# Kernel tuning notes

Measured on AMD Instinct MI355X. Metric: run time of the kernel, lower is better.

Reference implementation:

```python
import jax, jax.numpy as jnp
import numpy as np

B, N, D = 2, 2048, 1024
H = 16                      # num_heads, head_dim = 64
E, K, CF = 4, 2, 1.0        # num_experts, top_k, capacity_factor
MLP_H = int(D * 4.0)        # dense Mlp hidden (mlp_ratio=4.0)
MOE_H = int(D * 0.25)       # expert hidden (hard-coded dim*0.25 in source)


def setup_inputs() -> dict:
    key = jax.random.key(0)
    ks = jax.random.split(key, 12)
    r = lambda k, shp, s=0.02: jax.random.normal(k, shp, jnp.float32) * s
    return dict(
        x=jax.random.normal(ks[0], (B, N, D), jnp.float32),
        noise=jax.random.normal(ks[1], (B, N, E), jnp.float32),
        ln1_g=jnp.ones((D,), jnp.float32), ln1_b=jnp.zeros((D,), jnp.float32),
        ln2_g=jnp.ones((D,), jnp.float32), ln2_b=jnp.zeros((D,), jnp.float32),
        w_qkv=r(ks[2], (3 * D, D)),
        w_proj=r(ks[3], (D, D)), b_proj=jnp.zeros((D,), jnp.float32),
        w_route=r(ks[4], (D, E), 0.05), b_route=jnp.zeros((E,), jnp.float32),
        w_noise=r(ks[5], (D, E), 0.05), b_noise=jnp.zeros((E,), jnp.float32),
        we1=r(ks[6], (E, D, MOE_H)), be1=jnp.zeros((E, MOE_H), jnp.float32),
        we2=r(ks[7], (E, MOE_H, D)), be2=jnp.zeros((E, D), jnp.float32),
        w_mlp1=r(ks[8], (D, MLP_H)), b_mlp1=jnp.zeros((MLP_H,), jnp.float32),
        w_mlp2=r(ks[9], (MLP_H, D)), b_mlp2=jnp.zeros((D,), jnp.float32),
    )


def _ln(x, g, b, eps=1e-5):
    mu = x.mean(-1, keepdims=True)
    var = ((x - mu) ** 2).mean(-1, keepdims=True)
    return (x - mu) * jax.lax.rsqrt(var + eps) * g + b


def _gelu(x):
    return jax.nn.gelu(x, approximate=False)  # torch nn.GELU default (erf)


def reference(x, noise, ln1_g, ln1_b, ln2_g, ln2_b, w_qkv, w_proj, b_proj,
              w_route, b_route, w_noise, b_noise, we1, be1, we2, be2,
              w_mlp1, b_mlp1, w_mlp2, b_mlp2):
    Bs, Ns, Ds = x.shape
    hd = Ds // H
    # --- attention branch ---
    x1 = _ln(x, ln1_g, ln1_b)
    qkv = (x1 @ w_qkv.T).reshape(Bs, Ns, 3, H, hd).transpose(2, 0, 3, 1, 4)
    q, k, v = qkv[0] * (hd ** -0.5), qkv[1], qkv[2]
    attn = jax.nn.softmax(jnp.einsum('bhnd,bhmd->bhnm', q, k), axis=-1)
    ao = jnp.einsum('bhnm,bhmd->bhnd', attn, v).transpose(0, 2, 1, 3).reshape(Bs, Ns, Ds)
    x = x + (ao @ w_proj.T + b_proj)
    # --- shared norm for mlp + moe ---
    x2 = _ln(x, ln2_g, ln2_b)
    # --- noisy top-k router ---
    logits = x2 @ w_route + b_route                  # [B,N,E]
    noisy = logits + noise * jax.nn.softplus(x2 @ w_noise + b_noise)
    topv, topi = jax.lax.top_k(noisy, K)             # [B,N,K]
    probs = jax.nn.softmax(topv, axis=-1)            # softmax over sparse logits == softmax over top-k
    T = Bs * Ns
    flat_x = x2.reshape(T, Ds)
    fidx = topi.reshape(T, K)
    rows = jnp.arange(T)[:, None]
    gate = jnp.zeros((T, E), noisy.dtype).at[rows, fidx].set(probs.reshape(T, K))
    capacity = int(T * K / E * CF)
    # --- capacity-limited dispatch / expert MLP / combine ---
    def dispatch(eid, W1, b1, W2, b2):
        mask = jnp.any(fidx == eid, axis=-1)                     # [T]
        order = jnp.argsort(jnp.logical_not(mask))               # stable: selected tokens first, in token order
        sel = order[:capacity]                                   # [C]
        valid = mask[sel].astype(flat_x.dtype)
        h = _gelu(flat_x[sel] @ W1 + b1)
        out = h @ W2 + b2
        w = gate[sel, eid] * valid
        return sel, out * w[:, None]
    sel, outw = jax.vmap(dispatch)(jnp.arange(E), we1, be1, we2, be2)   # [E,C], [E,C,D]
    moe = jnp.zeros_like(flat_x).at[sel.reshape(-1)].add(outw.reshape(-1, Ds)).reshape(Bs, Ns, Ds)
    # --- dense mlp branch ---
    mlp = _gelu(x2 @ w_mlp1 + b_mlp1) @ w_mlp2 + b_mlp2
    return x + mlp + moe
```

## Files before the change

kernel.cpp:

```cpp
#include <hip/hip_runtime.h>
#include <hip/hip_bf16.h>
#include <math.h>

typedef __bf16 bf16;
typedef __bf16 bf16x4 __attribute__((ext_vector_type(4)));
typedef __bf16 bf16x8 __attribute__((ext_vector_type(8)));
typedef float  f32x4  __attribute__((ext_vector_type(4)));
typedef short  s16x4  __attribute__((ext_vector_type(4)));

#define T_TOK 4096
#define DIM   1024
#define NHEAD 16
#define SEQ   2048
#define NEXP  4
#define CAP   2048
#define MLPH  4096
#define MOEH  256

__device__ __forceinline__ float gelu_exact(float v) {
    return 0.5f * v * (1.f + erff(v * 0.70710678118654752f));
}

struct HL { bf16 h, l; };
__device__ __forceinline__ HL split2(float v) {
    HL r; r.h = (bf16)v; r.l = (bf16)(v - (float)r.h); return r;
}

__device__ __forceinline__ float fast_exp2(float x) {
#if __has_builtin(__builtin_amdgcn_exp2f)
    return __builtin_amdgcn_exp2f(x);
#else
    return exp2f(x);
#endif
}

__device__ __forceinline__ f32x4 mfma16(bf16x4 a, bf16x4 b, f32x4 c) {
    return __builtin_amdgcn_mfma_f32_16x16x16bf16_1k(
        __builtin_bit_cast(s16x4, a), __builtin_bit_cast(s16x4, b), c, 0, 0, 0);
}

__device__ __forceinline__ void gload16(const bf16* gptr, bf16* lptr) {
    __builtin_amdgcn_global_load_lds(
        (const __attribute__((address_space(1))) unsigned int*)gptr,
        (__attribute__((address_space(3))) unsigned int*)lptr,
        16, 0, 0);
}

__global__ __launch_bounds__(256)
void ln_split_kernel(const float* __restrict__ x, const float* __restrict__ g,
                     const float* __restrict__ b, bf16* __restrict__ oh, bf16* __restrict__ ol) {
    int wave = threadIdx.x >> 6, lane = threadIdx.x & 63;
    long t = (long)blockIdx.x * 4 + wave;
    const float* xr = x + t * DIM;
    float v[16];
    #pragma unroll
    for (int i = 0; i < 16; i++) v[i] = xr[i * 64 + lane];
    float s = 0.f, s2 = 0.f;
    #pragma unroll
    for (int i = 0; i < 16; i++) { s += v[i]; s2 += v[i] * v[i]; }
    #pragma unroll
    for (int m = 1; m < 64; m <<= 1) { s += __shfl_xor(s, m); s2 += __shfl_xor(s2, m); }
    float mu  = s * (1.f / DIM);
    float var = s2 * (1.f / DIM) - mu * mu;
    float rs  = 1.f / sqrtf(var + 1e-5f);
    #pragma unroll
    for (int i = 0; i < 16; i++) {
        int d = i * 64 + lane;
        HL sp = split2((v[i] - mu) * rs * g[d] + b[d]);
        oh[t * DIM + d] = sp.h; ol[t * DIM + d] = sp.l;
    }
}

__global__ __launch_bounds__(256)
void ln_kernel(const float* __restrict__ x, const float* __restrict__ g,
               const float* __restrict__ b, bf16* __restrict__ out) {
    int wave = threadIdx.x >> 6, lane = threadIdx.x & 63;
    long t = (long)blockIdx.x * 4 + wave;
    const float* xr = x + t * DIM;
    float v[16];
    #pragma unroll
    for (int i = 0; i < 16; i++) v[i] = xr[i * 64 + lane];
    float s = 0.f, s2 = 0.f;
    #pragma unroll
    for (int i = 0; i < 16; i++) { s += v[i]; s2 += v[i] * v[i]; }
    #pragma unroll
    for (int m = 1; m < 64; m <<= 1) { s += __shfl_xor(s, m); s2 += __shfl_xor(s2, m); }
    float mu  = s * (1.f / DIM);
    float var = s2 * (1.f / DIM) - mu * mu;
    float rs  = 1.f / sqrtf(var + 1e-5f);
    #pragma unroll
    for (int i = 0; i < 16; i++) {
        int d = i * 64 + lane;
        out[t * DIM + d] = (bf16)((v[i] - mu) * rs * g[d] + b[d]);
    }
}

__global__ __launch_bounds__(256)
void split_pair_kernel(const float* __restrict__ in, bf16* __restrict__ h, bf16* __restrict__ l) {
    long i0 = ((long)blockIdx.x * 256 + threadIdx.x) * 4;
    f32x4 v = *(const f32x4*)&in[i0];
    bf16x4 vh, vl;
    #pragma unroll
    for (int j = 0; j < 4; j++) { HL sp = split2(v[j]); vh[j] = sp.h; vl[j] = sp.l; }
    *(bf16x4*)&h[i0] = vh; *(bf16x4*)&l[i0] = vl;
}

__global__ __launch_bounds__(256)
void transpose_conv_kernel(const float* __restrict__ in, bf16* __restrict__ out, int R, int C) {
    __shared__ bf16 tile[32][33];
    long bo = (long)blockIdx.z * R * C;
    in += bo; out += bo;
    int c0 = blockIdx.x * 32, r0 = blockIdx.y * 32;
    int tx = threadIdx.x & 31, ty = threadIdx.x >> 5;
    #pragma unroll
    for (int i = 0; i < 32; i += 8)
        tile[ty + i][tx] = (bf16)in[(long)(r0 + ty + i) * C + c0 + tx];
    __syncthreads();
    #pragma unroll
    for (int i = 0; i < 32; i += 8)
        out[(long)(c0 + ty + i) * R + r0 + tx] = tile[tx][ty + i];
}

__global__ __launch_bounds__(256)
void gemm_qkv(const bf16* __restrict__ Ah_g, const bf16* __restrict__ Al_g,
              const bf16* __restrict__ Bh_g, const bf16* __restrict__ Bl_g,
              bf16* __restrict__ Qh_g, bf16* __restrict__ Ql_g,
              bf16* __restrict__ Kh_g, bf16* __restrict__ Kl_g,
              bf16* __restrict__ VtH, bf16* __restrict__ VtL) {
    const int K = DIM;
    __shared__ alignas(16) bf16 Ah[8192], Al[8192], Bh[8192], Bl[8192];
    int tid = threadIdx.x;
    int wave = tid >> 6, lane = tid & 63;
    int l16 = lane & 15, l4 = lane >> 4;
    int wr = (wave >> 1) * 64, wc = (wave & 1) * 64;
    int row0 = blockIdx.y * 128, col0 = blockIdx.x * 128;
    int colb = (lane & 7) * 8;
    f32x4 acc[4][4] = {};
    for (int k0 = 0; k0 < K; k0 += 64) {
        #pragma unroll
        for (int p = 0; p < 4; p++) {
            int rl = p * 32 + wave * 8 + (lane >> 3);
            int lb = p * 2048 + wave * 512;
            gload16(&Ah_g[(long)(row0 + rl) * K + k0 + colb], &Ah[lb]);
            gload16(&Al_g[(long)(row0 + rl) * K + k0 + colb], &Al[lb]);
            gload16(&Bh_g[(long)(col0 + rl) * K + k0 + colb], &Bh[lb]);
            gload16(&Bl_g[(long)(col0 + rl) * K + k0 + colb], &Bl[lb]);
        }
        __syncthreads();
        #pragma unroll
        for (int ks = 0; ks < 2; ks++) {
            bf16x8 ah[4], al[4], bh[4], bl[4];
            #pragma unroll
            for (int i = 0; i < 4; i++) {
                ah[i] = *(const bf16x8*)&Ah[(wr + i*16 + l16)*64 + ks*32 + l4*8];
                al[i] = *(const bf16x8*)&Al[(wr + i*16 + l16)*64 + ks*32 + l4*8];
            }
            #pragma unroll
            for (int j = 0; j < 4; j++) {
                bh[j] = *(const bf16x8*)&Bh[(wc + j*16 + l16)*64 + ks*32 + l4*8];
                bl[j] = *(const bf16x8*)&Bl[(wc + j*16 + l16)*64 + ks*32 + l4*8];
            }
            #pragma unroll
            for (int i = 0; i < 4; i++)
                #pragma unroll
                for (int j = 0; j < 4; j++) {
                    acc[i][j] = __builtin_amdgcn_mfma_f32_16x16x32_bf16(ah[i], bh[j], acc[i][j], 0, 0, 0);
                    acc[i][j] = __builtin_amdgcn_mfma_f32_16x16x32_bf16(ah[i], bl[j], acc[i][j], 0, 0, 0);
                    acc[i][j] = __builtin_amdgcn_mfma_f32_16x16x32_bf16(al[i], bh[j], acc[i][j], 0, 0, 0);
                }
        }
        __syncthreads();
    }
    if (col0 < 2048) {
        bf16* oh = (col0 < 1024) ? Qh_g : Kh_g;
        bf16* ol = (col0 < 1024) ? Ql_g : Kl_g;
        float qscale = (col0 < 1024) ? 0.18033688011112043f : 1.0f;
        #pragma unroll
        for (int i = 0; i < 4; i++)
            #pragma unroll
            for (int r = 0; r < 4; r++) {
                int t = row0 + wr + i * 16 + l4 * 4 + r;
                int bq = t >> 11, s = t & 2047;
                #pragma unroll
                for (int j = 0; j < 4; j++) {
                    int col = (col0 + wc + j * 16 + l16) & 1023;
                    int hh = col >> 6, dl = col & 63;
                    long o = ((long)(bq * NHEAD + hh) * SEQ + s) * 64 + dl;
                    HL sp = split2(acc[i][j][r] * qscale);
                    oh[o] = sp.h; ol[o] = sp.l;
                }
            }
    } else {
        #pragma unroll
        for (int i = 0; i < 4; i++) {
            int s0 = row0 + wr + i * 16 + l4 * 4;
            int b = s0 >> 11, sl = s0 & 2047;
            #pragma unroll
            for (int j = 0; j < 4; j++) {
                int d = col0 - 2048 + wc + j * 16 + l16;
                int h = d >> 6, dl = d & 63;
                long base = ((long)(b * NHEAD + h) * 64 + dl) * SEQ + (sl ^ ((dl & 1) << 2));
                bf16x4 vh, vl;
                #pragma unroll
                for (int r = 0; r < 4; r++) { HL sp = split2(acc[i][j][r]); vh[r] = sp.h; vl[r] = sp.l; }
                *(bf16x4*)&VtH[base] = vh;
                *(bf16x4*)&VtL[base] = vl;
            }
        }
    }
}

__device__ __forceinline__ bf16x8 sw_frag(const bf16* arr, int row, int cc) {
    return *(const bf16x8*)&arr[row * 64 + ((cc ^ (row & 7)) * 8)];
}
__device__ __forceinline__ bf16x4 v_frag(const bf16* arr, int d, int q) {
    return *(const bf16x4*)&arr[d * 64 + ((q ^ (d & 15)) * 4)];
}

__global__ __launch_bounds__(512, 4)
void flash_attn(const bf16* __restrict__ Qh_g, const bf16* __restrict__ Ql_g,
                const bf16* __restrict__ Kh_g, const bf16* __restrict__ Kl_g,
                const bf16* __restrict__ VtH_g, const bf16* __restrict__ VtL_g,
                bf16* __restrict__ aoh, bf16* __restrict__ aol) {
    __shared__ alignas(16) bf16 KhS[2][4096], KlS[2][4096], VhS[2][4096], VlS[2][4096];
    int tid = threadIdx.x;
    int wave = tid >> 6, lane = tid & 63;
    int l16 = lane & 15, l4 = lane >> 4;
    int bid = blockIdx.x;
    int bh = bid & 31;
    int b = bh >> 4, h = bh & 15;
    int q0 = (bid >> 5) * 128;

    bf16x8 qfh[2], qfl[2];
    {
        const bf16* qh = Qh_g + ((long)bh * SEQ + q0 + wave * 16 + l16) * 64;
        const bf16* ql = Ql_g + ((long)bh * SEQ + q0 + wave * 16 + l16) * 64;
        #pragma unroll
        for (int ks = 0; ks < 2; ks++) {
            qfh[ks] = *(const bf16x8*)&qh[ks * 32 + l4 * 8];
            qfl[ks] = *(const bf16x8*)&ql[ks * 32 + l4 * 8];
        }
    }
    int r8 = lane >> 3;
    int c8 = lane & 7;
    const bf16* kh_g = Kh_g + (long)bh * SEQ * 64;
    const bf16* kl_g = Kl_g + (long)bh * SEQ * 64;
    const bf16* vh_g = VtH_g + (long)bh * 64 * SEQ;
    const bf16* vl_g = VtL_g + (long)bh * 64 * SEQ;

    float m_s = -1e30f, l_s = 0.f;
    f32x4 accO[4] = {};

    auto stage = [&](int c0, int bsel) {
        int R0 = wave * 8;
        int row = R0 + r8;
        int ksw = (c8 ^ r8) * 8;
        int vsw = (c8 ^ ((wave * 4 + (r8 >> 1)) & 7)) * 8;
        gload16(&kh_g[(long)(c0 + row) * 64 + ksw], &KhS[bsel][R0 * 64]);
        gload16(&kl_g[(long)(c0 + row) * 64 + ksw], &KlS[bsel][R0 * 64]);
        gload16(&vh_g[(long)row * SEQ + c0 + vsw], &VhS[bsel][R0 * 64]);
        gload16(&vl_g[(long)row * SEQ + c0 + vsw], &VlS[bsel][R0 * 64]);
    };

    auto compute = [&](const bf16* KhT, const bf16* KlT, const bf16* VhT, const bf16* VlT) {
        f32x4 st[4] = {};
        __builtin_amdgcn_s_setprio(1);
        #pragma unroll
        for (int ks = 0; ks < 2; ks++) {
            #pragma unroll
            for (int i = 0; i < 4; i++) {
                bf16x8 akh = sw_frag(KhT, i * 16 + l16, ks * 4 + l4);
                bf16x8 akl = sw_frag(KlT, i * 16 + l16, ks * 4 + l4);
                st[i] = __builtin_amdgcn_mfma_f32_16x16x32_bf16(akh, qfh[ks], st[i], 0, 0, 0);
                st[i] = __builtin_amdgcn_mfma_f32_16x16x32_bf16(akl, qfh[ks], st[i], 0, 0, 0);
                st[i] = __builtin_amdgcn_mfma_f32_16x16x32_bf16(akh, qfl[ks], st[i], 0, 0, 0);
            }
        }
        __builtin_amdgcn_s_setprio(0);
        float mx = st[0][0];
        #pragma unroll
        for (int i = 0; i < 4; i++)
            #pragma unroll
            for (int r = 0; r < 4; r++) mx = fmaxf(mx, st[i][r]);
        mx = fmaxf(mx, __shfl_xor(mx, 16));
        mx = fmaxf(mx, __shfl_xor(mx, 32));
        if (!__all(mx <= m_s + 8.f)) {
            float mnew = fmaxf(m_s, mx);
            float alpha = fast_exp2(m_s - mnew);
            l_s *= alpha;
            #pragma unroll
            for (int i = 0; i < 4; i++)
                #pragma unroll
                for (int r = 0; r < 4; r++) accO[i][r] *= alpha;
            m_s = mnew;
        }
        float psum = 0.f;
        bf16x4 ph[4], pl[4];
        #pragma unroll
        for (int kb = 0; kb < 4; kb++)
            #pragma unroll
            for (int r = 0; r < 4; r++) {
                float pv = fast_exp2(st[kb][r] - m_s);
                psum += pv;
                HL sp = split2(pv);
                ph[kb][r] = sp.h; pl[kb][r] = sp.l;
            }
        psum += __shfl_xor(psum, 16);
        psum += __shfl_xor(psum, 32);
        l_s += psum;
        __builtin_amdgcn_s_setprio(1);
        #pragma unroll
        for (int kb = 0; kb < 4; kb++) {
            #pragma unroll
            for (int i = 0; i < 4; i++) {
                bf16x4 avh = v_frag(VhT, i * 16 + l16, kb * 4 + l4);
                bf16x4 avl = v_frag(VlT, i * 16 + l16, kb * 4 + l4);
                accO[i] = mfma16(avh, ph[kb], accO[i]);
                accO[i] = mfma16(avh, pl[kb], accO[i]);
                accO[i] = mfma16(avl, ph[kb], accO[i]);
            }
        }
        __builtin_amdgcn_s_setprio(0);
    };

    const int NT = SEQ / 64;
    stage(0, 0);
    #pragma unroll 1
    for (int t = 0; t < NT; t += 2) {
        stage((t + 1) * 64, 1);
        asm volatile("s_waitcnt vmcnt(4)" ::: "memory");
        __builtin_amdgcn_sched_barrier(0);
        __builtin_amdgcn_s_barrier();
        compute(KhS[0], KlS[0], VhS[0], VlS[0]);
        asm volatile("" ::: "memory");
        __builtin_amdgcn_s_barrier();
        if (t + 2 < NT) {
            stage((t + 2) * 64, 0);
            asm volatile("s_waitcnt vmcnt(4)" ::: "memory");
        } else {
            asm volatile("s_waitcnt vmcnt(0)" ::: "memory");
        }
        __builtin_amdgcn_sched_barrier(0);
        __builtin_amdgcn_s_barrier();
        compute(KhS[1], KlS[1], VhS[1], VlS[1]);
        asm volatile("" ::: "memory");
        __builtin_amdgcn_s_barrier();
    }

    float inv = 1.f / l_s;
    int q = q0 + wave * 16 + l16;
    #pragma unroll
    for (int i = 0; i < 4; i++) {
        bf16x4 oh4, ol4;
        #pragma unroll
        for (int r = 0; r < 4; r++) { HL sp = split2(accO[i][r] * inv); oh4[r] = sp.h; ol4[r] = sp.l; }
        long o = ((long)(b * SEQ + q)) * DIM + h * 64 + i * 16 + l4 * 4;
        *(bf16x4*)&aoh[o] = oh4;
        *(bf16x4*)&aol[o] = ol4;
    }
}

__global__ __launch_bounds__(256)
void gemm_proj(const bf16* __restrict__ Ah_g, const bf16* __restrict__ Al_g,
               const bf16* __restrict__ Bh_g, const bf16* __restrict__ Bl_g,
               const float* __restrict__ bias, const float* __restrict__ res,
               float* __restrict__ C, int N, int K) {
    __shared__ alignas(16) bf16 Ah[8192], Al[8192], Bh[8192], Bl[8192];
    int tid = threadIdx.x;
    int wave = tid >> 6, lane = tid & 63;
    int l16 = lane & 15, l4 = lane >> 4;
    int wr = (wave >> 1) * 64, wc = (wave & 1) * 64;
    int row0 = blockIdx.y * 128, col0 = blockIdx.x * 128;
    int colb = (lane & 7) * 8;
    f32x4 acc[4][4] = {};
    for (int k0 = 0; k0 < K; k0 += 64) {
        #pragma unroll
        for (int p = 0; p < 4; p++) {
            int rl = p * 32 + wave * 8 + (lane >> 3);
            int lb = p * 2048 + wave * 512;
            gload16(&Ah_g[(long)(row0 + rl) * K + k0 + colb], &Ah[lb]);
            gload16(&Al_g[(long)(row0 + rl) * K + k0 + colb], &Al[lb]);
            gload16(&Bh_g[(long)(col0 + rl) * K + k0 + colb], &Bh[lb]);
            gload16(&Bl_g[(long)(col0 + rl) * K + k0 + colb], &Bl[lb]);
        }
        __syncthreads();
        #pragma unroll
        for (int ks = 0; ks < 2; ks++) {
            bf16x8 ah[4], al[4], bh[4], bl[4];
            #pragma unroll
            for (int i = 0; i < 4; i++) {
                ah[i] = *(const bf16x8*)&Ah[(wr + i*16 + l16)*64 + ks*32 + l4*8];
                al[i] = *(const bf16x8*)&Al[(wr + i*16 + l16)*64 + ks*32 + l4*8];
            }
            #pragma unroll
            for (int j = 0; j < 4; j++) {
                bh[j] = *(const bf16x8*)&Bh[(wc + j*16 + l16)*64 + ks*32 + l4*8];
                bl[j] = *(const bf16x8*)&Bl[(wc + j*16 + l16)*64 + ks*32 + l4*8];
            }
            #pragma unroll
            for (int i = 0; i < 4; i++)
                #pragma unroll
                for (int j = 0; j < 4; j++) {
                    acc[i][j] = __builtin_amdgcn_mfma_f32_16x16x32_bf16(ah[i], bh[j], acc[i][j], 0, 0, 0);
                    acc[i][j] = __builtin_amdgcn_mfma_f32_16x16x32_bf16(ah[i], bl[j], acc[i][j], 0, 0, 0);
                    acc[i][j] = __builtin_amdgcn_mfma_f32_16x16x32_bf16(al[i], bh[j], acc[i][j], 0, 0, 0);
                }
        }
        __syncthreads();
    }
    #pragma unroll
    for (int i = 0; i < 4; i++)
        #pragma unroll
        for (int r = 0; r < 4; r++) {
            int grow = row0 + wr + i * 16 + l4 * 4 + r;
            #pragma unroll
            for (int j = 0; j < 4; j++) {
                int gcol = col0 + wc + j * 16 + l16;
                long o = (long)grow * N + gcol;
                C[o] = acc[i][j][r] + bias[gcol] + res[o];
            }
        }
}

template<bool BIAS, bool GELU, bool GATHER, int OUT_MODE>
__global__ __launch_bounds__(256)
void gemm_bt(const bf16* __restrict__ A, const bf16* __restrict__ Bt,
             const float* __restrict__ bias,
             bf16* __restrict__ Cbf, float* __restrict__ Cf,
             const int* __restrict__ rowmap, const float* __restrict__ roww,
             int M, int N, int K,
             long eA, long eB, long ebias, long eMap, long eC) {
    int ez = blockIdx.z;
    A += (long)ez * eA; Bt += (long)ez * eB;
    if (BIAS) bias += (long)ez * ebias;
    if (GATHER || OUT_MODE == 3) rowmap += (long)ez * eMap;
    if (OUT_MODE == 3) roww += (long)ez * eMap;
    if (OUT_MODE == 0) Cbf += (long)ez * eC;

    __shared__ alignas(16) bf16 As[8192];
    __shared__ alignas(16) bf16 Bs[8192];
    int tid = threadIdx.x;
    int wave = tid >> 6, lane = tid & 63;
    int l16 = lane & 15, l4 = lane >> 4;
    int wr = (wave >> 1) * 64, wc = (wave & 1) * 64;
    int row0 = blockIdx.y * 128, col0 = blockIdx.x * 128;
    int colb = (lane & 7) * 8;

    long arow[4];
    #pragma unroll
    for (int p = 0; p < 4; p++) {
        long gr = row0 + p * 32 + wave * 8 + (lane >> 3);
        if (GATHER) gr = rowmap[gr];
        arow[p] = gr;
    }
    f32x4 acc[4][4] = {};
    for (int k0 = 0; k0 < K; k0 += 64) {
        #pragma unroll
        for (int p = 0; p < 4; p++) {
            int rl = p * 32 + wave * 8 + (lane >> 3);
            int lb = p * 2048 + wave * 512;
            gload16(&A[arow[p] * K + k0 + colb], &As[lb]);
            gload16(&Bt[(long)(col0 + rl) * K + k0 + colb], &Bs[lb]);
        }
        __syncthreads();
        #pragma unroll
        for (int ks = 0; ks < 2; ks++) {
            bf16x8 af[4], bfr[4];
            #pragma unroll
            for (int i = 0; i < 4; i++) af[i]  = *(const bf16x8*)&As[(wr + i*16 + l16)*64 + ks*32 + l4*8];
            #pragma unroll
            for (int j = 0; j < 4; j++) bfr[j] = *(const bf16x8*)&Bs[(wc + j*16 + l16)*64 + ks*32 + l4*8];
            #pragma unroll
            for (int i = 0; i < 4; i++)
                #pragma unroll
                for (int j = 0; j < 4; j++)
                    acc[i][j] = __builtin_amdgcn_mfma_f32_16x16x32_bf16(af[i], bfr[j], acc[i][j], 0, 0, 0);
        }
        __syncthreads();
    }
    #pragma unroll
    for (int i = 0; i < 4; i++)
        #pragma unroll
        for (int r = 0; r < 4; r++) {
            int grow = row0 + wr + i * 16 + l4 * 4 + r;
            int st = 0; float sw = 0.f;
            if (OUT_MODE == 3) { st = rowmap[grow]; sw = roww[grow]; }
            #pragma unroll
            for (int j = 0; j < 4; j++) {
                int gcol = col0 + wc + j * 16 + l16;
                float v = acc[i][j][r];
                if (BIAS) v += bias[gcol];
                if (GELU) v = gelu_exact(v);
                if (OUT_MODE == 0) {
                    Cbf[(long)grow * N + gcol] = (bf16)v;
                } else if (OUT_MODE == 2) {
                    long o = (long)grow * N + gcol;
                    Cf[o] += v;
                } else {
                    atomicAdd(&Cf[(long)st * N + gcol], sw * v);
                }
            }
        }
}

__global__ __launch_bounds__(256)
void routing_kernel(const float* __restrict__ xres, const float* __restrict__ g,
                    const float* __restrict__ b, const float* __restrict__ w_route,
                    const float* __restrict__ b_route, const float* __restrict__ w_noise,
                    const float* __restrict__ b_noise, const float* __restrict__ noise,
                    int* __restrict__ topi, float* __restrict__ topp) {
    int wave = threadIdx.x >> 6, lane = threadIdx.x & 63;
    long t = (long)blockIdx.x * 4 + wave;
    const float* xr = xres + t * DIM;
    float v[16];
    #pragma unroll
    for (int i = 0; i < 16; i++) v[i] = xr[i * 64 + lane];
    float s = 0.f, s2 = 0.f;
    #pragma unroll
    for (int i = 0; i < 16; i++) { s += v[i]; s2 += v[i] * v[i]; }
    #pragma unroll
    for (int m = 1; m < 64; m <<= 1) { s += __shfl_xor(s, m); s2 += __shfl_xor(s2, m); }
    float mu  = s * (1.f / DIM);
    float var = s2 * (1.f / DIM) - mu * mu;
    float rs  = 1.f / sqrtf(var + 1e-5f);
    float accr[4] = {0.f,0.f,0.f,0.f}, accn[4] = {0.f,0.f,0.f,0.f};
    #pragma unroll
    for (int i = 0; i < 16; i++) {
        int d = i * 64 + lane;
        float n = (v[i] - mu) * rs * g[d] + b[d];
        #pragma unroll
        for (int e = 0; e < 4; e++) {
            accr[e] += n * w_route[d * 4 + e];
            accn[e] += n * w_noise[d * 4 + e];
        }
    }
    #pragma unroll
    for (int e = 0; e < 4; e++)
        #pragma unroll
        for (int m = 1; m < 64; m <<= 1) {
            accr[e] += __shfl_xor(accr[e], m);
            accn[e] += __shfl_xor(accn[e], m);
        }
    if (lane == 0) {
        float nz[4];
        #pragma unroll
        for (int e = 0; e < 4; e++) {
            float logit = accr[e] + b_route[e];
            float si = accn[e] + b_noise[e];
            float sp = si > 0.f ? si + log1pf(expf(-si)) : log1pf(expf(si));
            nz[e] = logit + noise[t * 4 + e] * sp;
        }
        int i1 = 0;
        #pragma unroll
        for (int e = 1; e < 4; e++) if (nz[e] > nz[i1]) i1 = e;
        int i2 = -1; float v2 = -1e30f;
        #pragma unroll
        for (int e = 0; e < 4; e++) if (e != i1 && nz[e] > v2) { v2 = nz[e]; i2 = e; }
        float ex = expf(v2 - nz[i1]);
        topi[t * 2]     = i1; topi[t * 2 + 1] = i2;
        topp[t * 2]     = 1.f / (1.f + ex);
        topp[t * 2 + 1] = ex / (1.f + ex);
    }
}

__global__ __launch_bounds__(256)
void dispatch_kernel(const int* __restrict__ topi, const float* __restrict__ topp,
                     int* __restrict__ sel, float* __restrict__ wgt) {
    int e = threadIdx.x >> 6, lane = threadIdx.x & 63;
    int cnt = 0;
    for (int c = 0; c < T_TOK; c += 64) {
        int t = c + lane;
        int i0 = topi[t * 2], i1 = topi[t * 2 + 1];
        bool m = (i0 == e) || (i1 == e);
        unsigned long long bal = __ballot(m);
        int pos = cnt + __popcll(bal & ((1ull << lane) - 1ull));
        if (m && pos < CAP) {
            sel[e * CAP + pos] = t;
            wgt[e * CAP + pos] = (i0 == e) ? topp[t * 2] : topp[t * 2 + 1];
        }
        cnt += (int)__popcll(bal);
    }
    if (cnt > CAP) cnt = CAP;
    for (int pos = cnt + lane; pos < CAP; pos += 64) {
        sel[e * CAP + pos] = 0;
        wgt[e * CAP + pos] = 0.f;
    }
}

extern "C" void kernel_launch(void* const* d_in, const int* in_sizes, int n_in,
                              void* d_out, int out_size, void* d_ws, size_t ws_size,
                              hipStream_t stream) {
    (void)in_sizes; (void)n_in; (void)out_size; (void)ws_size;
    const float* x       = (const float*)d_in[0];
    const float* noise   = (const float*)d_in[1];
    const float* ln1_g   = (const float*)d_in[2];
    const float* ln1_b   = (const float*)d_in[3];
    const float* ln2_g   = (const float*)d_in[4];
    const float* ln2_b   = (const float*)d_in[5];
    const float* w_qkv   = (const float*)d_in[6];
    const float* w_proj  = (const float*)d_in[7];
    const float* b_proj  = (const float*)d_in[8];
    const float* w_route = (const float*)d_in[9];
    const float* b_route = (const float*)d_in[10];
    const float* w_noise = (const float*)d_in[11];
    const float* b_noise = (const float*)d_in[12];
    const float* we1     = (const float*)d_in[13];
    const float* be1     = (const float*)d_in[14];
    const float* we2     = (const float*)d_in[15];
    const float* be2     = (const float*)d_in[16];
    const float* w_mlp1  = (const float*)d_in[17];
    const float* b_mlp1  = (const float*)d_in[18];
    const float* w_mlp2  = (const float*)d_in[19];
    const float* b_mlp2  = (const float*)d_in[20];
    float* d_outf = (float*)d_out;

    const size_t MB = 1024 * 1024;
    char* ws = (char*)d_ws;
    bf16* x1h = (bf16*)(ws);
    bf16* x1l = (bf16*)(ws + 8 * MB);
    bf16* aoh = (bf16*)(ws);
    bf16* aol = (bf16*)(ws + 8 * MB);
    bf16* w_mlp1T = (bf16*)(ws);
    bf16* w_mlp2T = (bf16*)(ws + 8 * MB);
    bf16* wqkvh = (bf16*)(ws + 16 * MB);
    bf16* wqkvl = (bf16*)(ws + 22 * MB);
    bf16* we1T  = (bf16*)(ws + 16 * MB);
    bf16* we2T  = (bf16*)(ws + 18 * MB);
    bf16* h_e   = (bf16*)(ws + 20 * MB);
    bf16* wprojh = (bf16*)(ws + 28 * MB);
    bf16* wprojl = (bf16*)(ws + 30 * MB);
    bf16* Qh = (bf16*)(ws + 32 * MB);
    bf16* Ql = (bf16*)(ws + 40 * MB);
    bf16* Kh = (bf16*)(ws + 48 * MB);
    bf16* Kl = (bf16*)(ws + 56 * MB);
    bf16* h_mlp = (bf16*)(ws + 32 * MB);
    bf16*  VtH  = (bf16*)(ws + 64 * MB);
    bf16*  VtL  = (bf16*)(ws + 72 * MB);
    bf16*  x2b  = (bf16*)(ws + 64 * MB);
    int*   topi = (int*)(ws + 72 * MB);
    float* topp = (float*)(ws + 72 * MB + 32768);
    int*   sel  = (int*)(ws + 72 * MB + 65536);
    float* wgt  = (float*)(ws + 72 * MB + 98304);

    ln_split_kernel<<<T_TOK/4, 256, 0, stream>>>(x, ln1_g, ln1_b, x1h, x1l);
    split_pair_kernel<<<(3*DIM*DIM)/1024, 256, 0, stream>>>(w_qkv, wqkvh, wqkvl);
    split_pair_kernel<<<(DIM*DIM)/1024,   256, 0, stream>>>(w_proj, wprojh, wprojl);

    gemm_qkv<<<dim3(3*DIM/128, T_TOK/128), 256, 0, stream>>>(
        x1h, x1l, wqkvh, wqkvl, Qh, Ql, Kh, Kl, VtH, VtL);

    flash_attn<<<dim3(32 * (SEQ/128)), 512, 0, stream>>>(Qh, Ql, Kh, Kl, VtH, VtL, aoh, aol);

    gemm_proj<<<dim3(DIM/128, T_TOK/128), 256, 0, stream>>>(
        aoh, aol, wprojh, wprojl, b_proj, x, d_outf, DIM, DIM);

    ln_kernel<<<T_TOK/4, 256, 0, stream>>>(d_outf, ln2_g, ln2_b, x2b);
    routing_kernel<<<T_TOK/4, 256, 0, stream>>>(d_outf, ln2_g, ln2_b, w_route, b_route,
                                                w_noise, b_noise, noise, topi, topp);
    dispatch_kernel<<<1, 256, 0, stream>>>(topi, topp, sel, wgt);

    transpose_conv_kernel<<<dim3(MLPH/32, DIM/32, 1),    256, 0, stream>>>(w_mlp1, w_mlp1T, DIM, MLPH);
    transpose_conv_kernel<<<dim3(DIM/32, MLPH/32, 1),    256, 0, stream>>>(w_mlp2, w_mlp2T, MLPH, DIM);
    transpose_conv_kernel<<<dim3(MOEH/32, DIM/32, NEXP), 256, 0, stream>>>(we1, we1T, DIM, MOEH);
    transpose_conv_kernel<<<dim3(DIM/32, MOEH/32, NEXP), 256, 0, stream>>>(we2, we2T, MOEH, DIM);

    gemm_bt<true,true,false,0><<<dim3(MLPH/128, T_TOK/128), 256, 0, stream>>>(
        x2b, w_mlp1T, b_mlp1, h_mlp, nullptr, nullptr, nullptr, T_TOK, MLPH, DIM,
        0, 0, 0, 0, 0);
    gemm_bt<true,false,false,2><<<dim3(DIM/128, T_TOK/128), 256, 0, stream>>>(
        h_mlp, w_mlp2T, b_mlp2, nullptr, d_outf, nullptr, nullptr, T_TOK, DIM, MLPH,
        0, 0, 0, 0, 0);

    gemm_bt<true,true,true,0><<<dim3(MOEH/128, CAP/128, NEXP), 256, 0, stream>>>(
        x2b, we1T, be1, h_e, nullptr, sel, nullptr, CAP, MOEH, DIM,
        0, (long)MOEH*DIM, MOEH, CAP, (long)CAP*MOEH);
    gemm_bt<true,false,false,3><<<dim3(DIM/128, CAP/128, NEXP), 256, 0, stream>>>(
        h_e, we2T, be2, nullptr, d_outf, sel, wgt, CAP, DIM, MOEH,
        (long)CAP*MOEH, (long)DIM*MOEH, DIM, CAP, 0);
}
```

Baseline: 681.1 us.

## Drop low-order Q and P split terms in attention; fuse LN2 into routing

Result: faster. 649.8 us (-4.6%).

```diff
diff --git a/kernel.cpp b/kernel.cpp
--- a/kernel.cpp
+++ b/kernel.cpp
@@ -68,30 +68,6 @@
         int d = i * 64 + lane;
         HL sp = split2((v[i] - mu) * rs * g[d] + b[d]);
         oh[t * DIM + d] = sp.h; ol[t * DIM + d] = sp.l;
-    }
-}
-
-__global__ __launch_bounds__(256)
-void ln_kernel(const float* __restrict__ x, const float* __restrict__ g,
-               const float* __restrict__ b, bf16* __restrict__ out) {
-    int wave = threadIdx.x >> 6, lane = threadIdx.x & 63;
-    long t = (long)blockIdx.x * 4 + wave;
-    const float* xr = x + t * DIM;
-    float v[16];
-    #pragma unroll
-    for (int i = 0; i < 16; i++) v[i] = xr[i * 64 + lane];
-    float s = 0.f, s2 = 0.f;
-    #pragma unroll
-    for (int i = 0; i < 16; i++) { s += v[i]; s2 += v[i] * v[i]; }
-    #pragma unroll
-    for (int m = 1; m < 64; m <<= 1) { s += __shfl_xor(s, m); s2 += __shfl_xor(s2, m); }
-    float mu  = s * (1.f / DIM);
-    float var = s2 * (1.f / DIM) - mu * mu;
-    float rs  = 1.f / sqrtf(var + 1e-5f);
-    #pragma unroll
-    for (int i = 0; i < 16; i++) {
-        int d = i * 64 + lane;
-        out[t * DIM + d] = (bf16)((v[i] - mu) * rs * g[d] + b[d]);
     }
 }
 
@@ -172,9 +148,10 @@
         __syncthreads();
     }
     if (col0 < 2048) {
-        bf16* oh = (col0 < 1024) ? Qh_g : Kh_g;
-        bf16* ol = (col0 < 1024) ? Ql_g : Kl_g;
-        float qscale = (col0 < 1024) ? 0.18033688011112043f : 1.0f;
+        bool isQ = (col0 < 1024);
+        bf16* oh = isQ ? Qh_g : Kh_g;
+        bf16* ol = isQ ? Ql_g : Kl_g;
+        float qscale = isQ ? 0.18033688011112043f : 1.0f;
         #pragma unroll
         for (int i = 0; i < 4; i++)
             #pragma unroll
@@ -187,7 +164,8 @@
                     int hh = col >> 6, dl = col & 63;
                     long o = ((long)(bq * NHEAD + hh) * SEQ + s) * 64 + dl;
                     HL sp = split2(acc[i][j][r] * qscale);
-                    oh[o] = sp.h; ol[o] = sp.l;
+                    oh[o] = sp.h;
+                    if (!isQ) ol[o] = sp.l;
                 }
             }
     } else {
@@ -218,7 +196,7 @@
 }
 
 __global__ __launch_bounds__(512, 4)
-void flash_attn(const bf16* __restrict__ Qh_g, const bf16* __restrict__ Ql_g,
+void flash_attn(const bf16* __restrict__ Qh_g,
                 const bf16* __restrict__ Kh_g, const bf16* __restrict__ Kl_g,
                 const bf16* __restrict__ VtH_g, const bf16* __restrict__ VtL_g,
                 bf16* __restrict__ aoh, bf16* __restrict__ aol) {
@@ -231,15 +209,12 @@
     int b = bh >> 4, h = bh & 15;
     int q0 = (bid >> 5) * 128;
 
-    bf16x8 qfh[2], qfl[2];
+    bf16x8 qfh[2];
     {
         const bf16* qh = Qh_g + ((long)bh * SEQ + q0 + wave * 16 + l16) * 64;
-        const bf16* ql = Ql_g + ((long)bh * SEQ + q0 + wave * 16 + l16) * 64;
-        #pragma unroll
-        for (int ks = 0; ks < 2; ks++) {
+        #pragma unroll
+        for (int ks = 0; ks < 2; ks++)
             qfh[ks] = *(const bf16x8*)&qh[ks * 32 + l4 * 8];
-            qfl[ks] = *(const bf16x8*)&ql[ks * 32 + l4 * 8];
-        }
     }
     int r8 = lane >> 3;
     int c8 = lane & 7;
@@ -273,7 +248,6 @@
                 bf16x8 akl = sw_frag(KlT, i * 16 + l16, ks * 4 + l4);
                 st[i] = __builtin_amdgcn_mfma_f32_16x16x32_bf16(akh, qfh[ks], st[i], 0, 0, 0);
                 st[i] = __builtin_amdgcn_mfma_f32_16x16x32_bf16(akl, qfh[ks], st[i], 0, 0, 0);
-                st[i] = __builtin_amdgcn_mfma_f32_16x16x32_bf16(akh, qfl[ks], st[i], 0, 0, 0);
             }
         }
         __builtin_amdgcn_s_setprio(0);
@@ -295,15 +269,14 @@
             m_s = mnew;
         }
         float psum = 0.f;
-        bf16x4 ph[4], pl[4];
+        bf16x4 ph[4];
         #pragma unroll
         for (int kb = 0; kb < 4; kb++)
             #pragma unroll
             for (int r = 0; r < 4; r++) {
                 float pv = fast_exp2(st[kb][r] - m_s);
                 psum += pv;
-                HL sp = split2(pv);
-                ph[kb][r] = sp.h; pl[kb][r] = sp.l;
+                ph[kb][r] = (bf16)pv;
             }
         psum += __shfl_xor(psum, 16);
         psum += __shfl_xor(psum, 32);
@@ -316,7 +289,6 @@
                 bf16x4 avh = v_frag(VhT, i * 16 + l16, kb * 4 + l4);
                 bf16x4 avl = v_frag(VlT, i * 16 + l16, kb * 4 + l4);
                 accO[i] = mfma16(avh, ph[kb], accO[i]);
-                accO[i] = mfma16(avh, pl[kb], accO[i]);
                 accO[i] = mfma16(avl, ph[kb], accO[i]);
             }
         }
@@ -508,7 +480,8 @@
                     const float* __restrict__ b, const float* __restrict__ w_route,
                     const float* __restrict__ b_route, const float* __restrict__ w_noise,
                     const float* __restrict__ b_noise, const float* __restrict__ noise,
-                    int* __restrict__ topi, float* __restrict__ topp) {
+                    int* __restrict__ topi, float* __restrict__ topp,
+                    bf16* __restrict__ x2b) {
     int wave = threadIdx.x >> 6, lane = threadIdx.x & 63;
     long t = (long)blockIdx.x * 4 + wave;
     const float* xr = xres + t * DIM;
@@ -528,6 +501,7 @@
     for (int i = 0; i < 16; i++) {
         int d = i * 64 + lane;
         float n = (v[i] - mu) * rs * g[d] + b[d];
+        x2b[t * DIM + d] = (bf16)n;
         #pragma unroll
         for (int e = 0; e < 4; e++) {
             accr[e] += n * w_route[d * 4 + e];
@@ -649,14 +623,13 @@
     gemm_qkv<<<dim3(3*DIM/128, T_TOK/128), 256, 0, stream>>>(
         x1h, x1l, wqkvh, wqkvl, Qh, Ql, Kh, Kl, VtH, VtL);
 
-    flash_attn<<<dim3(32 * (SEQ/128)), 512, 0, stream>>>(Qh, Ql, Kh, Kl, VtH, VtL, aoh, aol);
+    flash_attn<<<dim3(32 * (SEQ/128)), 512, 0, stream>>>(Qh, Kh, Kl, VtH, VtL, aoh, aol);
 
     gemm_proj<<<dim3(DIM/128, T_TOK/128), 256, 0, stream>>>(
         aoh, aol, wprojh, wprojl, b_proj, x, d_outf, DIM, DIM);
 
-    ln_kernel<<<T_TOK/4, 256, 0, stream>>>(d_outf, ln2_g, ln2_b, x2b);
     routing_kernel<<<T_TOK/4, 256, 0, stream>>>(d_outf, ln2_g, ln2_b, w_route, b_route,
-                                                w_noise, b_noise, noise, topi, topp);
+                                                w_noise, b_noise, noise, topi, topp, x2b);
     dispatch_kernel<<<1, 256, 0, stream>>>(topi, topp, sel, wgt);
 
     transpose_conv_kernel<<<dim3(MLPH/32, DIM/32, 1),    256, 0, stream>>>(w_mlp1, w_mlp1T, DIM, MLPH);
```
